# Performance work log

Measured on AMD Instinct MI355X. Metric: run time of the kernel, lower is better.

## Reference

```python
import jax, jax.numpy as jnp
import numpy as np

N = 1_048_576          # number of samples
NUM_CLASSES = 128      # C
NUM_SUBGROUPS = 4      # S


def setup_inputs() -> dict:
    key = jax.random.key(0)
    k1, k2, k3 = jax.random.split(key, 3)
    logits = jax.random.normal(k1, (N, NUM_CLASSES), dtype=jnp.float32)
    targets = jax.random.randint(k2, (N,), 0, NUM_CLASSES, dtype=jnp.int64)
    subgroup_inf = jax.random.randint(k3, (N,), 0, NUM_SUBGROUPS, dtype=jnp.int64)
    return {"logits": logits, "targets": targets, "subgroup_inf": subgroup_inf}


def reference(logits, targets, subgroup_inf):
    # per-sample cross-entropy, reduction='none'
    logp = jax.nn.log_softmax(logits, axis=-1)                      # [N, C]
    per_sample = -jnp.take_along_axis(logp, targets[:, None], axis=1)[:, 0]  # [N]

    # group id for the (y, s) pair; counts via one scatter-add histogram
    group_id = targets * NUM_SUBGROUPS + subgroup_inf               # [N]
    counts = jax.ops.segment_sum(
        jnp.ones_like(per_sample), group_id,
        num_segments=NUM_CLASSES * NUM_SUBGROUPS)                   # [C*S]

    # loss[mask] /= mask.sum()  ==  divide each sample by its group's count
    weighted = per_sample / counts[group_id]                        # [N]
    return weighted.sum()
```

## Files before the change

kernel.cpp:

```cpp
#include <hip/hip_runtime.h>

#define NCLS 128
#define NSUB 4
#define NGRP (NCLS * NSUB)
#define MAIN_BLOCKS 2048
#define MAIN_THREADS 256
#define HIST_BLOCKS 256
#define HIST_THREADS 256


__global__ void orl_zero_kernel(int* __restrict__ counts) {
    int i = threadIdx.x;
    if (i < NGRP) counts[i] = 0;
}

__global__ void orl_hist_kernel(const int* __restrict__ tgt,
                                const int* __restrict__ sub,
                                int* __restrict__ counts, int n4) {
    __shared__ int h[NGRP];
    for (int i = threadIdx.x; i < NGRP; i += blockDim.x) h[i] = 0;
    __syncthreads();
    const int tid = blockIdx.x * blockDim.x + threadIdx.x;
    const int stride = gridDim.x * blockDim.x;
    const int4* t4 = (const int4*)tgt;
    const int4* s4 = (const int4*)sub;
    for (int i = tid; i < n4; i += stride) {
        int4 t = t4[i];
        int4 s = s4[i];
        atomicAdd(&h[(t.x << 2) | s.x], 1);
        atomicAdd(&h[(t.y << 2) | s.y], 1);
        atomicAdd(&h[(t.z << 2) | s.z], 1);
        atomicAdd(&h[(t.w << 2) | s.w], 1);
    }
    __syncthreads();
    for (int i = threadIdx.x; i < NGRP; i += blockDim.x) {
        int v = h[i];
        if (v) atomicAdd(&counts[i], v);
    }
}

__global__ void orl_recip_kernel(const int* __restrict__ counts,
                                 float* __restrict__ recip) {
    int i = threadIdx.x;
    if (i < NGRP) {
        int c = counts[i];
        recip[i] = c ? (1.0f / (float)c) : 0.0f;
    }
}

__global__ void orl_main_kernel(const float* __restrict__ logits,
                                const int* __restrict__ tgt,
                                const int* __restrict__ sub,
                                const float* __restrict__ recip,
                                double* __restrict__ partials, int n) {
    const int lane  = threadIdx.x & 63;
    const int wid   = threadIdx.x >> 6;
    const int gwave = (blockIdx.x * blockDim.x + threadIdx.x) >> 6;
    const int nwave = (gridDim.x * blockDim.x) >> 6;

    float local = 0.0f;
    for (int row = gwave; row < n; row += nwave) {
        const float2 v = reinterpret_cast<const float2*>(logits)[(size_t)row * 64 + lane];
        float m = fmaxf(v.x, v.y);
        #pragma unroll
        for (int off = 32; off; off >>= 1) m = fmaxf(m, __shfl_xor(m, off));
        float e = __expf(v.x - m) + __expf(v.y - m);
        #pragma unroll
        for (int off = 32; off; off >>= 1) e += __shfl_xor(e, off);
        int t = tgt[row];
        float cand = (t & 1) ? v.y : v.x;
        float tv = __shfl(cand, t >> 1);
        float ps = m + __logf(e) - tv;
        int g = (t << 2) | sub[row];
        local += ps * recip[g];
    }

    __shared__ float wsum[MAIN_THREADS / 64];
    if (lane == 0) wsum[wid] = local;
    __syncthreads();
    if (threadIdx.x == 0) {
        double b = 0.0;
        #pragma unroll
        for (int w = 0; w < MAIN_THREADS / 64; ++w) b += (double)wsum[w];
        partials[blockIdx.x] = b;
    }
}

__global__ void orl_final_kernel(const double* __restrict__ partials, int nb,
                                 float* __restrict__ out) {
    double v = 0.0;
    for (int i = threadIdx.x; i < nb; i += blockDim.x) v += partials[i];
    #pragma unroll
    for (int off = 32; off; off >>= 1) v += __shfl_xor(v, off);
    __shared__ double sm[4];
    const int lane = threadIdx.x & 63, wid = threadIdx.x >> 6;
    if (lane == 0) sm[wid] = v;
    __syncthreads();
    if (threadIdx.x == 0) out[0] = (float)(sm[0] + sm[1] + sm[2] + sm[3]);
}

extern "C" void kernel_launch(void* const* d_in, const int* in_sizes, int n_in,
                              void* d_out, int out_size, void* d_ws, size_t ws_size,
                              hipStream_t stream) {
    const float* logits = (const float*)d_in[0];
    const int*   tgt    = (const int*)d_in[1];
    const int*   sub    = (const int*)d_in[2];
    const int n = in_sizes[1];

    int*    counts   = (int*)d_ws;
    float*  recip    = (float*)((char*)d_ws + NGRP * sizeof(int));
    double* partials = (double*)((char*)d_ws + 8192);
    float*  out      = (float*)d_out;

    orl_zero_kernel<<<1, NGRP, 0, stream>>>(counts);
    orl_hist_kernel<<<HIST_BLOCKS, HIST_THREADS, 0, stream>>>(tgt, sub, counts, n / 4);
    orl_recip_kernel<<<1, NGRP, 0, stream>>>(counts, recip);
    orl_main_kernel<<<MAIN_BLOCKS, MAIN_THREADS, 0, stream>>>(logits, tgt, sub, recip, partials, n);
    orl_final_kernel<<<1, 256, 0, stream>>>(partials, MAIN_BLOCKS, out);
}
```

Measured before the change: 725.8 us.

## Process eight rows per wavefront with float4 loads and fold reciprocal into main kernel

The main kernel now assigns eight rows to each wavefront, with eight lanes per row. Each lane loads four float4 values and reduces 16 elements in registers, so each row needs only three cross-lane shuffle steps instead of six, and the loads are wider. The separate reciprocal kernel is removed and the main kernel divides by the raw count directly, which saves one launch. In exchange, each lane needs more registers, and the row count is assumed to be divisible by eight.

```diff
diff --git a/kernel.cpp b/kernel.cpp
--- a/kernel.cpp
+++ b/kernel.cpp
@@ -1,4 +1,5 @@
 #include <hip/hip_runtime.h>
+
 
 #define NCLS 128
 #define NSUB 4
@@ -39,44 +40,62 @@
     }
 }
 
-__global__ void orl_recip_kernel(const int* __restrict__ counts,
-                                 float* __restrict__ recip) {
-    int i = threadIdx.x;
-    if (i < NGRP) {
-        int c = counts[i];
-        recip[i] = c ? (1.0f / (float)c) : 0.0f;
-    }
-}
-
 __global__ void orl_main_kernel(const float* __restrict__ logits,
                                 const int* __restrict__ tgt,
                                 const int* __restrict__ sub,
-                                const float* __restrict__ recip,
-                                double* __restrict__ partials, int n) {
-    const int lane  = threadIdx.x & 63;
-    const int wid   = threadIdx.x >> 6;
-    const int gwave = (blockIdx.x * blockDim.x + threadIdx.x) >> 6;
-    const int nwave = (gridDim.x * blockDim.x) >> 6;
+                                const int* __restrict__ counts,
+                                double* __restrict__ partials, int n8) {
+    const int lane = threadIdx.x & 63;
+    const int sl   = lane & 7;
+    const int grp  = lane >> 3;
+    const int wid  = threadIdx.x >> 6;
+    const int gw   = (blockIdx.x * blockDim.x + threadIdx.x) >> 6;
+    const int nw   = (gridDim.x * blockDim.x) >> 6;
+    const int sl4  = sl << 2;
 
     float local = 0.0f;
-    for (int row = gwave; row < n; row += nwave) {
-        const float2 v = reinterpret_cast<const float2*>(logits)[(size_t)row * 64 + lane];
-        float m = fmaxf(v.x, v.y);
+    for (int rb = gw; rb < n8; rb += nw) {
+        const int row = (rb << 3) + grp;
+        const float4* rp = reinterpret_cast<const float4*>(logits + ((size_t)row << 7));
+        float4 A = rp[sl];
+        float4 B = rp[sl + 8];
+        float4 C = rp[sl + 16];
+        float4 D = rp[sl + 24];
+        const int t = tgt[row];
+        const int s = sub[row];
+
+        float v[16] = {A.x, A.y, A.z, A.w, B.x, B.y, B.z, B.w,
+                       C.x, C.y, C.z, C.w, D.x, D.y, D.z, D.w};
+        float m = v[0];
         #pragma unroll
-        for (int off = 32; off; off >>= 1) m = fmaxf(m, __shfl_xor(m, off));
-        float e = __expf(v.x - m) + __expf(v.y - m);
+        for (int k = 1; k < 16; ++k) m = fmaxf(m, v[k]);
+        m = fmaxf(m, __shfl_xor(m, 1));
+        m = fmaxf(m, __shfl_xor(m, 2));
+        m = fmaxf(m, __shfl_xor(m, 4));
+
+        const int tt = t - sl4;
+        float e = 0.0f, tv = 0.0f;
         #pragma unroll
-        for (int off = 32; off; off >>= 1) e += __shfl_xor(e, off);
-        int t = tgt[row];
-        float cand = (t & 1) ? v.y : v.x;
-        float tv = __shfl(cand, t >> 1);
-        float ps = m + __logf(e) - tv;
-        int g = (t << 2) | sub[row];
-        local += ps * recip[g];
+        for (int k = 0; k < 16; ++k) {
+            e += __expf(v[k] - m);
+            const int code = ((k >> 2) << 5) + (k & 3);
+            tv = (code == tt) ? v[k] : tv;
+        }
+        e  += __shfl_xor(e, 1);  tv += __shfl_xor(tv, 1);
+        e  += __shfl_xor(e, 2);  tv += __shfl_xor(tv, 2);
+        e  += __shfl_xor(e, 4);  tv += __shfl_xor(tv, 4);
+
+        const float ps = m + __logf(e) - tv;
+        const int cnt = counts[(t << 2) | s];
+        const float w = ps / (float)cnt;
+        if (sl == 0) local += w;
     }
 
+    #pragma unroll
+    for (int off = 32; off; off >>= 1) local += __shfl_xor(local, off);
+
     __shared__ float wsum[MAIN_THREADS / 64];
-    if (lane == 0) wsum[wid] = local;
+    if ((threadIdx.x & 63) == 0) wsum[wid] = local;
     __syncthreads();
     if (threadIdx.x == 0) {
         double b = 0.0;
@@ -108,13 +127,11 @@
     const int n = in_sizes[1];
 
     int*    counts   = (int*)d_ws;
-    float*  recip    = (float*)((char*)d_ws + NGRP * sizeof(int));
     double* partials = (double*)((char*)d_ws + 8192);
     float*  out      = (float*)d_out;
 
     orl_zero_kernel<<<1, NGRP, 0, stream>>>(counts);
     orl_hist_kernel<<<HIST_BLOCKS, HIST_THREADS, 0, stream>>>(tgt, sub, counts, n / 4);
-    orl_recip_kernel<<<1, NGRP, 0, stream>>>(counts, recip);
-    orl_main_kernel<<<MAIN_BLOCKS, MAIN_THREADS, 0, stream>>>(logits, tgt, sub, recip, partials, n);
+    orl_main_kernel<<<MAIN_BLOCKS, MAIN_THREADS, 0, stream>>>(logits, tgt, sub, counts, partials, n >> 3);
     orl_final_kernel<<<1, 256, 0, stream>>>(partials, MAIN_BLOCKS, out);
 }
```

After: 689.0 us. -5.1%, faster.
